# Kernel tuning notes

Hardware: AMD Instinct MI355X
Metric: run time of the kernel (lower is better)

The kernel has to match this reference:

```python
import jax, jax.numpy as jnp
import numpy as np

B, N, D = 2, 2048, 768
H = 12
HD = D // H
HID = 4 * D
SCALE = HD ** -0.5
EPS = 1e-5


def layer_norm(x, g, b):
    mu = jnp.mean(x, axis=-1, keepdims=True)
    var = jnp.var(x, axis=-1, keepdims=True)
    return (x - mu) * jax.lax.rsqrt(var + EPS) * g + b


def setup_inputs() -> dict:
    key = jax.random.key(0)
    ks = jax.random.split(key, 12)
    s = 0.02
    return {
        "x": jax.random.normal(ks[0], (B, N, D), jnp.float32),
        "att_mask": jax.random.randint(ks[1], (B, N), 0, 2, jnp.int32),
        "ln1_g": jnp.ones((D,), jnp.float32),
        "ln1_b": jnp.zeros((D,), jnp.float32),
        "qkv_w": jax.random.normal(ks[2], (3 * D, D), jnp.float32) * s,
        "q_bias": jnp.zeros((D,), jnp.float32),
        "v_bias": jnp.zeros((D,), jnp.float32),
        "proj_w": jax.random.normal(ks[3], (D, D), jnp.float32) * s,
        "proj_b": jnp.zeros((D,), jnp.float32),
        "ln2_g": jnp.ones((D,), jnp.float32),
        "ln2_b": jnp.zeros((D,), jnp.float32),
        "fc1_w": jax.random.normal(ks[4], (HID, D), jnp.float32) * s,
        "fc1_b": jnp.zeros((HID,), jnp.float32),
        "fc2_w": jax.random.normal(ks[5], (D, HID), jnp.float32) * s,
        "fc2_b": jnp.zeros((D,), jnp.float32),
        "gamma_1": 0.1 * jnp.ones((D,), jnp.float32),
        "gamma_2": 0.1 * jnp.ones((D,), jnp.float32),
    }


def reference(x, att_mask, ln1_g, ln1_b, qkv_w, q_bias, v_bias, proj_w, proj_b,
              ln2_g, ln2_b, fc1_w, fc1_b, fc2_w, fc2_b, gamma_1, gamma_2):
    # --- attention branch ---
    h = layer_norm(x, ln1_g, ln1_b)
    qkv_bias = jnp.concatenate([q_bias, jnp.zeros_like(v_bias), v_bias])
    qkv = h @ qkv_w.T + qkv_bias                      # [B,N,3D]
    qkv = qkv.reshape(B, N, 3, H, HD).transpose(2, 0, 3, 1, 4)
    q, k, v = qkv[0], qkv[1], qkv[2]                  # [B,H,N,HD]
    logit = jnp.einsum('bhqd,bhkd->bhqk', q * SCALE, k)
    mask = att_mask[:, None, None, :]                 # key mask [B,1,1,N]
    logit = jnp.where(mask == 0, -jnp.inf, logit)
    attn = jax.nn.softmax(logit, axis=-1)
    o = jnp.einsum('bhqk,bhkd->bhqd', attn, v)
    o = o.transpose(0, 2, 1, 3).reshape(B, N, D)
    o = o @ proj_w.T + proj_b
    x = x + gamma_1 * o
    # --- mlp branch ---
    h2 = layer_norm(x, ln2_g, ln2_b)
    h2 = jax.nn.gelu(h2 @ fc1_w.T + fc1_b, approximate=False)
    h2 = h2 @ fc2_w.T + fc2_b
    return x + gamma_2 * h2
```

## Files before the change

kernel.cpp:

```cpp
#include <hip/hip_runtime.h>
#include <hip/hip_bf16.h>
#include <stdint.h>

typedef __bf16 bf16x8 __attribute__((ext_vector_type(8)));
typedef __bf16 bf16x2 __attribute__((ext_vector_type(2)));
typedef unsigned short u16x8 __attribute__((ext_vector_type(8)));
typedef float f32x4 __attribute__((ext_vector_type(4)));
typedef float f32x16 __attribute__((ext_vector_type(16)));
typedef uint32_t u32x4 __attribute__((ext_vector_type(4)));

#define DMODEL 768
#define NSEQ   2048
#define BATCH  2
#define NHEAD  12
#define HDIM   64
#define HIDDEN 3072
#define PROWS  (BATCH * NHEAD * NSEQ)
#define QSCALE 0.18033688011112042f
#define MCONST 16.0f
#define PMASKED 1.52587890625e-05f

__device__ __forceinline__ uint16_t f2bf(float f) {
  __bf16 h = (__bf16)f;
  return __builtin_bit_cast(uint16_t, h);
}
__device__ __forceinline__ float bf2f(uint16_t u) {
  uint32_t x = (uint32_t)u << 16;
  return __builtin_bit_cast(float, x);
}
__device__ __forceinline__ bf16x8 ldb8(const uint16_t* p) {
  return __builtin_bit_cast(bf16x8, *reinterpret_cast<const u16x8*>(p));
}

using as1_void = __attribute__((address_space(1))) const void;
using as3_void = __attribute__((address_space(3))) void;
__device__ __forceinline__ void gload16(const uint16_t* src, uint16_t* lds) {
  __builtin_amdgcn_global_load_lds((as1_void*)src, (as3_void*)lds, 16, 0, 0);
}
#define MEMFENCE asm volatile("" ::: "memory")

#define N_QKVW  (3 * DMODEL * DMODEL)
#define N_PROJW (DMODEL * DMODEL)
#define N_FC1W  (HIDDEN * DMODEL)
#define N_FC2W  (DMODEL * HIDDEN)
__global__ __launch_bounds__(256) void cvt4_kernel(const float* __restrict__ s0,
                                                   const float* __restrict__ s1,
                                                   const float* __restrict__ s2,
                                                   const float* __restrict__ s3,
                                                   uint16_t* __restrict__ d0,
                                                   uint16_t* __restrict__ d1,
                                                   uint16_t* __restrict__ d2,
                                                   uint16_t* __restrict__ d3) {
  int i4 = (blockIdx.x * 256 + threadIdx.x) * 4;
  const float* s;
  uint16_t* d;
  if (i4 < N_QKVW) { s = s0 + i4; d = d0 + i4; }
  else if (i4 < N_QKVW + N_PROJW) { int j = i4 - N_QKVW; s = s1 + j; d = d1 + j; }
  else if (i4 < N_QKVW + N_PROJW + N_FC1W) { int j = i4 - N_QKVW - N_PROJW; s = s2 + j; d = d2 + j; }
  else { int j = i4 - N_QKVW - N_PROJW - N_FC1W; s = s3 + j; d = d3 + j; }
  float4 v = *reinterpret_cast<const float4*>(s);
  ushort4 o;
  o.x = f2bf(v.x); o.y = f2bf(v.y); o.z = f2bf(v.z); o.w = f2bf(v.w);
  *reinterpret_cast<ushort4*>(d) = o;
}

__global__ __launch_bounds__(256) void bias_kernel(const float* __restrict__ qb,
                                                   const float* __restrict__ vb,
                                                   float* __restrict__ out) {
  int j = blockIdx.x * 256 + threadIdx.x;
  if (j < 3 * DMODEL) {
    float v = 0.f;
    if (j < DMODEL) v = qb[j];
    else if (j >= 2 * DMODEL) v = vb[j - 2 * DMODEL];
    out[j] = v;
  }
}

__global__ __launch_bounds__(256) void ln_kernel(const float* __restrict__ x,
                                                 const float* __restrict__ g,
                                                 const float* __restrict__ bt,
                                                 uint16_t* __restrict__ out) {
  const int row = blockIdx.x;
  const int t = threadIdx.x;
  const float* xr = x + (size_t)row * DMODEL;
  float v0 = xr[t], v1 = xr[t + 256], v2 = xr[t + 512];
  float s = v0 + v1 + v2;
  float q = v0 * v0 + v1 * v1 + v2 * v2;
  for (int off = 32; off >= 1; off >>= 1) {
    s += __shfl_xor(s, off);
    q += __shfl_xor(q, off);
  }
  __shared__ float ss[4], sq[4];
  int w = t >> 6;
  if ((t & 63) == 0) { ss[w] = s; sq[w] = q; }
  __syncthreads();
  s = ss[0] + ss[1] + ss[2] + ss[3];
  q = sq[0] + sq[1] + sq[2] + sq[3];
  const float mean = s * (1.0f / DMODEL);
  const float var = q * (1.0f / DMODEL) - mean * mean;
  const float rstd = rsqrtf(var + 1e-5f);
  uint16_t* orow = out + (size_t)row * DMODEL;
  orow[t]       = f2bf((v0 - mean) * rstd * g[t]       + bt[t]);
  orow[t + 256] = f2bf((v1 - mean) * rstd * g[t + 256] + bt[t + 256]);
  orow[t + 512] = f2bf((v2 - mean) * rstd * g[t + 512] + bt[t + 512]);
}

template <int MODE>
__global__ __launch_bounds__(256, 3) void gemm128(const uint16_t* __restrict__ A,
                                                  const uint16_t* __restrict__ W,
                                                  const float* __restrict__ bias,
                                                  void* __restrict__ outp,
                                                  int M, int N, int K) {
  __shared__ uint16_t As[2][128 * 32];
  __shared__ uint16_t Bs[2][128 * 32];
  const int tid = threadIdx.x;
  const int lane = tid & 63;
  const int w = tid >> 6;
  const int wr = w >> 1, wc = w & 1;
  const int row0 = blockIdx.y * 128;
  const int col0 = blockIdx.x * 128;
  const int lr = lane & 15;
  const int g = lane >> 4;

  const int o0 = w * 1024 + lane * 16;
  const int o1 = o0 + 4096;
  const int r0s = o0 >> 6, c0s = (o0 & 63) >> 1;
  const int r1s = o1 >> 6, c1s = (o1 & 63) >> 1;
  const int l0 = (w * 1024) >> 1;
  const int l1 = l0 + 2048;
  const uint16_t* Abase = A + (size_t)row0 * K;
  const uint16_t* Wbase = W + (size_t)col0 * K;

  auto stage = [&](int kt) {
    uint16_t* Ad = &As[kt & 1][0];
    uint16_t* Bd = &Bs[kt & 1][0];
    const int kk = kt * 32;
    gload16(Abase + (size_t)r0s * K + kk + c0s, Ad + l0);
    gload16(Abase + (size_t)r1s * K + kk + c1s, Ad + l1);
    gload16(Wbase + (size_t)r0s * K + kk + c0s, Bd + l0);
    gload16(Wbase + (size_t)r1s * K + kk + c1s, Bd + l1);
  };

  f32x4 acc[4][4] = {};
  const int nt = K >> 5;
  stage(0);
  for (int kt = 0; kt < nt; ++kt) {
    if (kt + 1 < nt) {
      stage(kt + 1);
      asm volatile("s_waitcnt vmcnt(4)" ::: "memory");
    } else {
      asm volatile("s_waitcnt vmcnt(0)" ::: "memory");
    }
    __builtin_amdgcn_s_barrier();
    MEMFENCE;
    const uint16_t* Ab = &As[kt & 1][0];
    const uint16_t* Bb = &Bs[kt & 1][0];
    bf16x8 a[4], b[4];
#pragma unroll
    for (int m = 0; m < 4; ++m) a[m] = ldb8(Ab + (wr * 64 + m * 16 + lr) * 32 + g * 8);
#pragma unroll
    for (int n = 0; n < 4; ++n) b[n] = ldb8(Bb + (wc * 64 + n * 16 + lr) * 32 + g * 8);
#pragma unroll
    for (int m = 0; m < 4; ++m)
#pragma unroll
      for (int n = 0; n < 4; ++n)
        acc[m][n] = __builtin_amdgcn_mfma_f32_16x16x32_bf16(a[m], b[n], acc[m][n], 0, 0, 0);
    MEMFENCE;
    __builtin_amdgcn_s_barrier();
  }

#pragma unroll
  for (int m = 0; m < 4; ++m) {
    int row = row0 + wr * 64 + m * 16 + g * 4;
#pragma unroll
    for (int n = 0; n < 4; ++n) {
      int col = col0 + wc * 64 + n * 16 + lr;
      float bv = bias[col];
#pragma unroll
      for (int ri = 0; ri < 4; ++ri) {
        float val = acc[m][n][ri] + bv;
        size_t idx = (size_t)(row + ri) * N + col;
        if constexpr (MODE == 0) {
          if (col < DMODEL) val *= QSCALE;
          ((uint16_t*)outp)[idx] = f2bf(val);
        } else {
          float ge = 0.5f * val * (1.0f + erff(val * 0.70710678118654752f));
          ((uint16_t*)outp)[idx] = f2bf(ge);
        }
      }
    }
  }
}

__global__ __launch_bounds__(256, 3) void gemm64(const uint16_t* __restrict__ A,
                                                 const uint16_t* __restrict__ W,
                                                 const float* __restrict__ bias,
                                                 float* __restrict__ outp,
                                                 const float* __restrict__ resid,
                                                 const float* __restrict__ gamma,
                                                 int M, int N, int K) {
  __shared__ uint16_t As[2][64 * 64];
  __shared__ uint16_t Bs[2][64 * 64];
  const int tid = threadIdx.x;
  const int lane = tid & 63;
  const int w = tid >> 6;
  const int wr = w >> 1, wc = w & 1;
  const int row0 = blockIdx.y * 64;
  const int col0 = blockIdx.x * 64;
  const int lr = lane & 15;
  const int g = lane >> 4;

  const int srow = tid >> 3;
  const int schunk = tid & 7;
  const uint16_t* Abase = A + (size_t)row0 * K;
  const uint16_t* Wbase = W + (size_t)col0 * K;

  auto stage = [&](int kt) {
    uint16_t* Ad = &As[kt & 1][0];
    uint16_t* Bd = &Bs[kt & 1][0];
    const int kk = kt * 64;
#pragma unroll
    for (int i = 0; i < 2; ++i) {
      const int row = i * 32 + srow;
      const int sc = (schunk ^ (row & 7)) * 8;
      gload16(Abase + (size_t)row * K + kk + sc, Ad + i * 2048 + w * 512);
      gload16(Wbase + (size_t)row * K + kk + sc, Bd + i * 2048 + w * 512);
    }
  };

  f32x4 acc[2][2] = {};
  const int nt = K >> 6;
  stage(0);
  for (int kt = 0; kt < nt; ++kt) {
    if (kt + 1 < nt) {
      stage(kt + 1);
      asm volatile("s_waitcnt vmcnt(4)" ::: "memory");
    } else {
      asm volatile("s_waitcnt vmcnt(0)" ::: "memory");
    }
    __builtin_amdgcn_s_barrier();
    MEMFENCE;
    const uint16_t* Ab = &As[kt & 1][0];
    const uint16_t* Bb = &Bs[kt & 1][0];
#pragma unroll
    for (int kk = 0; kk < 2; ++kk) {
      bf16x8 a[2], bf[2];
#pragma unroll
      for (int m = 0; m < 2; ++m) {
        const int row = wr * 32 + m * 16 + lr;
        a[m] = ldb8(Ab + row * 64 + (((kk * 4 + g) ^ (row & 7)) * 8));
      }
#pragma unroll
      for (int n = 0; n < 2; ++n) {
        const int row = wc * 32 + n * 16 + lr;
        bf[n] = ldb8(Bb + row * 64 + (((kk * 4 + g) ^ (row & 7)) * 8));
      }
#pragma unroll
      for (int m = 0; m < 2; ++m)
#pragma unroll
        for (int n = 0; n < 2; ++n)
          acc[m][n] = __builtin_amdgcn_mfma_f32_16x16x32_bf16(a[m], bf[n], acc[m][n], 0, 0, 0);
    }
    MEMFENCE;
    __builtin_amdgcn_s_barrier();
  }

#pragma unroll
  for (int m = 0; m < 2; ++m) {
    int row = row0 + wr * 32 + m * 16 + g * 4;
#pragma unroll
    for (int n = 0; n < 2; ++n) {
      int col = col0 + wc * 32 + n * 16 + lr;
      float bv = bias[col];
      float gv = gamma[col];
#pragma unroll
      for (int ri = 0; ri < 4; ++ri) {
        float val = acc[m][n][ri] + bv;
        size_t idx = (size_t)(row + ri) * N + col;
        outp[idx] = resid[idx] + gv * val;
      }
    }
  }
}

__global__ __launch_bounds__(256) void prep_kernel(const uint16_t* __restrict__ qkv,
                                                   const int* __restrict__ mask,
                                                   uint16_t* __restrict__ km,
                                                   uint16_t* __restrict__ vt) {
  __shared__ uint16_t tile[64][72];
  const int t = threadIdx.x;
  const int bh = blockIdx.x;
  const int n0 = blockIdx.y * 64;
  const int b = bh / NHEAD, h = bh % NHEAD;
  const int* mb = mask + b * NSEQ;
  const uint16_t* src = qkv + (size_t)(b * NSEQ + n0) * (3 * DMODEL) + h * HDIM;
  uint16_t* kdst = km + (size_t)(b * NSEQ + n0) * DMODEL + h * HDIM;
#pragma unroll
  for (int it = 0; it < 2; ++it) {
    int slot = it * 256 + t;
    int r = slot >> 2, c = (slot & 3) * 16;
    uint16_t mz = (mb[n0 + r] != 0) ? (uint16_t)0xFFFF : (uint16_t)0;
    const uint16_t* rp = src + (size_t)r * (3 * DMODEL);
    u16x8 k0 = *reinterpret_cast<const u16x8*>(rp + DMODEL + c) & mz;
    u16x8 k1 = *reinterpret_cast<const u16x8*>(rp + DMODEL + c + 8) & mz;
    u16x8 v0 = *reinterpret_cast<const u16x8*>(rp + 2 * DMODEL + c) & mz;
    u16x8 v1 = *reinterpret_cast<const u16x8*>(rp + 2 * DMODEL + c + 8) & mz;
    *reinterpret_cast<u16x8*>(kdst + (size_t)r * DMODEL + c) = k0;
    *reinterpret_cast<u16x8*>(kdst + (size_t)r * DMODEL + c + 8) = k1;
    *reinterpret_cast<u16x8*>(&tile[r][c]) = v0;
    *reinterpret_cast<u16x8*>(&tile[r][c + 8]) = v1;
  }
  __syncthreads();
  uint16_t* dst = vt + (size_t)bh * HDIM * NSEQ + n0;
#pragma unroll
  for (int it = 0; it < 2; ++it) {
    int slot = it * 256 + t;
    int d = slot >> 2, c = (slot & 3) * 16;
    u16x8 a0, a1;
#pragma unroll
    for (int e = 0; e < 8; ++e) a0[e] = tile[c + e][d];
#pragma unroll
    for (int e = 0; e < 8; ++e) a1[e] = tile[c + 8 + e][d];
    *reinterpret_cast<u16x8*>(dst + (size_t)d * NSEQ + c) = a0;
    *reinterpret_cast<u16x8*>(dst + (size_t)d * NSEQ + c + 8) = a1;
  }
}

__global__ __launch_bounds__(256, 3) void attn_kernel(const uint16_t* __restrict__ qkv,
                                                      const uint16_t* __restrict__ km,
                                                      const uint16_t* __restrict__ vt,
                                                      const int* __restrict__ mask,
                                                      uint16_t* __restrict__ po,
                                                      float* __restrict__ pml) {
  __shared__ uint16_t Kb[2][64 * 64];
  __shared__ uint16_t Vb[2][64 * 64];
  __shared__ unsigned long long mbits[16];
  const int tid = threadIdx.x;
  const int lane = tid & 63;
  const int w = tid >> 6;
  const int bh = blockIdx.x;
  const int b = bh / NHEAD, hd = bh % NHEAD;
  const int z = blockIdx.z;
  const int kbase = z * 1024;
  const int q0 = blockIdx.y * 128 + w * 32;
  const int l31 = lane & 31;
  const int hh = lane >> 5;

  const int* mb = mask + b * NSEQ;
#pragma unroll
  for (int it = 0; it < 4; ++it) {
    unsigned long long bm = __ballot(mb[kbase + it * 256 + tid] != 0);
    if (lane == 0) mbits[it * 4 + w] = bm;
  }

  bf16x8 qa[4];
  const uint16_t* qptr = qkv + (size_t)(b * NSEQ + q0 + l31) * (3 * DMODEL) + hd * HDIM + hh * 8;
#pragma unroll
  for (int dblk = 0; dblk < 4; ++dblk) qa[dblk] = ldb8(qptr + dblk * 16);

  const uint16_t* kmb = km + (size_t)b * NSEQ * DMODEL + hd * HDIM;
  const uint16_t* vtb = vt + (size_t)bh * HDIM * NSEQ;

  __syncthreads();

  const int srow = tid >> 3;
  const int sxor = ((tid & 7) ^ (srow & 7)) * 8;
  auto stage = [&](int t) {
    const int pb = t & 1;
    const int k0 = kbase + t * 64;
#pragma unroll
    for (int i = 0; i < 2; ++i) {
      const int row = i * 32 + srow;
      gload16(kmb + (size_t)(k0 + row) * DMODEL + sxor, &Kb[pb][i * 2048 + w * 512]);
      gload16(vtb + (size_t)row * NSEQ + k0 + sxor, &Vb[pb][i * 2048 + w * 512]);
    }
  };

  u16x8 ones_u;
#pragma unroll
  for (int e = 0; e < 8; ++e) ones_u[e] = 0x3F80;
  const bf16x8 ones = __builtin_bit_cast(bf16x8, ones_u);

  f32x16 oacc[2] = {};
  f32x16 lacc = {};

  stage(0);
  for (int t = 0; t < 16; ++t) {
    if (t + 1 < 16) {
      stage(t + 1);
      asm volatile("s_waitcnt vmcnt(4)" ::: "memory");
    } else {
      asm volatile("s_waitcnt vmcnt(0)" ::: "memory");
    }
    __builtin_amdgcn_s_barrier();
    MEMFENCE;
    const uint16_t* Kbp = &Kb[t & 1][0];
    const uint16_t* Vbp = &Vb[t & 1][0];

    f32x16 st[2];
    __builtin_amdgcn_s_setprio(1);
#pragma unroll
    for (int kblk = 0; kblk < 2; ++kblk) {
      f32x16 acc = {};
      const uint16_t* kr = Kbp + (kblk * 32 + l31) * 64;
#pragma unroll
      for (int dblk = 0; dblk < 4; ++dblk) {
        bf16x8 kf = ldb8(kr + ((dblk * 2 + hh) ^ (l31 & 7)) * 8);
        acc = __builtin_amdgcn_mfma_f32_32x32x16_bf16(kf, qa[dblk], acc, 0, 0, 0);
      }
      st[kblk] = acc;
    }
    __builtin_amdgcn_s_setprio(0);

    uint32_t pk[2][8];
#pragma unroll
    for (int kblk = 0; kblk < 2; ++kblk)
#pragma unroll
      for (int wn = 0; wn < 8; ++wn) {
        float e0 = exp2f(st[kblk][2 * wn] - MCONST);
        float e1 = exp2f(st[kblk][2 * wn + 1] - MCONST);
        bf16x2 pr = {(__bf16)e0, (__bf16)e1};
        pk[kblk][wn] = __builtin_bit_cast(uint32_t, pr);
      }

    bf16x8 af[4];
#pragma unroll
    for (int kb16 = 0; kb16 < 4; ++kb16) {
      const int kblk = kb16 >> 1;
      const int a4 = (kb16 & 1) * 4;
      uint32_t ow0 = hh ? pk[kblk][a4 + 2] : pk[kblk][a4 + 0];
      uint32_t ow1 = hh ? pk[kblk][a4 + 3] : pk[kblk][a4 + 1];
      uint32_t gv0 = hh ? pk[kblk][a4 + 0] : pk[kblk][a4 + 2];
      uint32_t gv1 = hh ? pk[kblk][a4 + 1] : pk[kblk][a4 + 3];
      uint32_t sw0 = (uint32_t)__shfl_xor((int)gv0, 32);
      uint32_t sw1 = (uint32_t)__shfl_xor((int)gv1, 32);
      u32x4 afu;
      afu[0] = hh ? sw0 : ow0;
      afu[1] = hh ? sw1 : ow1;
      afu[2] = hh ? ow0 : sw0;
      afu[3] = hh ? ow1 : sw1;
      af[kb16] = __builtin_bit_cast(bf16x8, afu);
    }

    __builtin_amdgcn_s_setprio(1);
#pragma unroll
    for (int dblk = 0; dblk < 2; ++dblk) {
      const uint16_t* vr = Vbp + (dblk * 32 + l31) * 64;
#pragma unroll
      for (int kb16 = 0; kb16 < 4; ++kb16) {
        bf16x8 vf = ldb8(vr + ((kb16 * 2 + hh) ^ (l31 & 7)) * 8);
        oacc[dblk] = __builtin_amdgcn_mfma_f32_32x32x16_bf16(af[kb16], vf, oacc[dblk], 0, 0, 0);
      }
    }
#pragma unroll
    for (int kb16 = 0; kb16 < 4; ++kb16)
      lacc = __builtin_amdgcn_mfma_f32_32x32x16_bf16(af[kb16], ones, lacc, 0, 0, 0);
    __builtin_amdgcn_s_setprio(0);
    MEMFENCE;
    __builtin_amdgcn_s_barrier();
  }

  int cnt = 0;
#pragma unroll
  for (int it = 0; it < 16; ++it) cnt += 64 - __popcll(mbits[it]);
  const float cntf = (float)cnt * PMASKED;

  uint16_t* ob = po + ((size_t)z * PROWS + (size_t)bh * NSEQ + q0) * 64;
#pragma unroll
  for (int r = 0; r < 16; ++r) {
    const int qrow = (r & 3) + 8 * (r >> 2) + 4 * hh;
#pragma unroll
    for (int dblk = 0; dblk < 2; ++dblk)
      ob[(size_t)qrow * 64 + dblk * 32 + l31] = f2bf(oacc[dblk][r]);
  }
  if (l31 == 0) {
#pragma unroll
    for (int r = 0; r < 16; ++r) {
      const int qrow = (r & 3) + 8 * (r >> 2) + 4 * hh;
      pml[(size_t)z * PROWS + (size_t)bh * NSEQ + q0 + qrow] = lacc[r] - cntf;
    }
  }
}

__global__ __launch_bounds__(256) void merge_kernel(const uint16_t* __restrict__ po,
                                                    const float* __restrict__ pml,
                                                    uint16_t* __restrict__ o) {
  int gid = blockIdx.x * 256 + threadIdx.x;
  int row = gid >> 3;
  int c0 = (gid & 7) * 8;
  float L = pml[row] + pml[PROWS + row];
  float inv = L > 0.f ? 1.f / L : 0.f;
  u16x8 a = *reinterpret_cast<const u16x8*>(po + (size_t)row * 64 + c0);
  u16x8 b = *reinterpret_cast<const u16x8*>(po + ((size_t)PROWS + row) * 64 + c0);
  int bh = row >> 11, q = row & 2047;
  int bb = bh / NHEAD, hh = bh % NHEAD;
  uint16_t* op = o + ((size_t)(bb * NSEQ + q) * DMODEL + hh * HDIM + c0);
  u16x8 outv;
#pragma unroll
  for (int e = 0; e < 8; ++e)
    outv[e] = f2bf((bf2f(a[e]) + bf2f(b[e])) * inv);
  *reinterpret_cast<u16x8*>(op) = outv;
}

extern "C" void kernel_launch(void* const* d_in, const int* in_sizes, int n_in,
                              void* d_out, int out_size, void* d_ws, size_t ws_size,
                              hipStream_t stream) {
  const float* x      = (const float*)d_in[0];
  const int*   amask  = (const int*)d_in[1];
  const float* ln1_g  = (const float*)d_in[2];
  const float* ln1_b  = (const float*)d_in[3];
  const float* qkv_w  = (const float*)d_in[4];
  const float* q_bias = (const float*)d_in[5];
  const float* v_bias = (const float*)d_in[6];
  const float* proj_w = (const float*)d_in[7];
  const float* proj_b = (const float*)d_in[8];
  const float* ln2_g  = (const float*)d_in[9];
  const float* ln2_b  = (const float*)d_in[10];
  const float* fc1_w  = (const float*)d_in[11];
  const float* fc1_b  = (const float*)d_in[12];
  const float* fc2_w  = (const float*)d_in[13];
  const float* fc2_b  = (const float*)d_in[14];
  const float* g1     = (const float*)d_in[15];
  const float* g2     = (const float*)d_in[16];

  char* ws = (char*)d_ws;
  uint16_t* qkvw_bf  = (uint16_t*)(ws + 0);
  uint16_t* projw_bf = (uint16_t*)(ws + 3538944);
  uint16_t* fc1w_bf  = (uint16_t*)(ws + 4718592);
  uint16_t* fc2w_bf  = (uint16_t*)(ws + 9437184);
  float*    qkvbias  = (float*)(ws + 14155776);
  uint16_t* h_bf     = (uint16_t*)(ws + 14164992);
  uint16_t* km       = h_bf;
  uint16_t* h2_bf    = h_bf;
  uint16_t* qkv_bf   = (uint16_t*)(ws + 20456448);
  uint16_t* vt_bf    = (uint16_t*)(ws + 39330816);
  uint16_t* o_bf     = (uint16_t*)(ws + 45622272);
  float*    x1_f     = (float*)(ws + 51913728);
  uint16_t* po       = (uint16_t*)(ws + 51913728);
  float*    pml      = (float*)(ws + 64496640);
  uint16_t* fc1_bf   = qkv_bf;

  const int M = BATCH * NSEQ;

  cvt4_kernel<<<(N_QKVW + N_PROJW + N_FC1W + N_FC2W) / 1024, 256, 0, stream>>>(
      qkv_w, proj_w, fc1_w, fc2_w, qkvw_bf, projw_bf, fc1w_bf, fc2w_bf);
  bias_kernel<<<(3 * DMODEL + 255) / 256, 256, 0, stream>>>(q_bias, v_bias, qkvbias);

  ln_kernel<<<M, 256, 0, stream>>>(x, ln1_g, ln1_b, h_bf);
  gemm128<0><<<dim3((3 * DMODEL) / 128, M / 128), 256, 0, stream>>>(
      h_bf, qkvw_bf, qkvbias, qkv_bf, M, 3 * DMODEL, DMODEL);
  prep_kernel<<<dim3(BATCH * NHEAD, NSEQ / 64), 256, 0, stream>>>(qkv_bf, amask, km, vt_bf);
  attn_kernel<<<dim3(BATCH * NHEAD, NSEQ / 128, 2), 256, 0, stream>>>(
      qkv_bf, km, vt_bf, amask, po, pml);
  merge_kernel<<<(PROWS * 8) / 256, 256, 0, stream>>>(po, pml, o_bf);
  gemm64<<<dim3(DMODEL / 64, M / 64), 256, 0, stream>>>(
      o_bf, projw_bf, proj_b, x1_f, x, g1, M, DMODEL, DMODEL);
  ln_kernel<<<M, 256, 0, stream>>>(x1_f, ln2_g, ln2_b, h2_bf);
  gemm128<2><<<dim3(HIDDEN / 128, M / 128), 256, 0, stream>>>(
      h2_bf, fc1w_bf, fc1_b, fc1_bf, M, HIDDEN, DMODEL);
  gemm64<<<dim3(DMODEL / 64, M / 64), 256, 0, stream>>>(
      fc1_bf, fc2w_bf, fc2_b, (float*)d_out, x1_f, g2, M, DMODEL, HIDDEN);
}
```

Before: 195.2 us.

## Fuse K/V masking and V transpose into QKV GEMM; split attention keys four ways

The QKV GEMM epilogue now writes Q, the masked K, and the masked, transposed V directly, which removes the separate prep kernel and its round trip through global memory. The attention kernel moves to 512-thread blocks covering 256 queries, and the key range is split into four chunks of 512 keys instead of two chunks of 1024. The merge kernel sums four partial outputs. The V-transpose stores from the GEMM epilogue are scattered 8-byte writes, and the four-way split adds more partial-output traffic in the merge.

```diff
diff --git a/kernel.cpp b/kernel.cpp
--- a/kernel.cpp
+++ b/kernel.cpp
@@ -16,6 +16,7 @@
 #define HDIM   64
 #define HIDDEN 3072
 #define PROWS  (BATCH * NHEAD * NSEQ)
+#define NZ     4
 #define QSCALE 0.18033688011112042f
 #define MCONST 16.0f
 #define PMASKED 1.52587890625e-05f
@@ -110,6 +111,9 @@
                                                   const uint16_t* __restrict__ W,
                                                   const float* __restrict__ bias,
                                                   void* __restrict__ outp,
+                                                  uint16_t* __restrict__ km,
+                                                  uint16_t* __restrict__ vt,
+                                                  const int* __restrict__ amask,
                                                   int M, int N, int K) {
   __shared__ uint16_t As[2][128 * 32];
   __shared__ uint16_t Bs[2][128 * 32];
@@ -169,23 +173,58 @@
     __builtin_amdgcn_s_barrier();
   }
 
-#pragma unroll
-  for (int m = 0; m < 4; ++m) {
-    int row = row0 + wr * 64 + m * 16 + g * 4;
-#pragma unroll
-    for (int n = 0; n < 4; ++n) {
-      int col = col0 + wc * 64 + n * 16 + lr;
-      float bv = bias[col];
-#pragma unroll
-      for (int ri = 0; ri < 4; ++ri) {
-        float val = acc[m][n][ri] + bv;
-        size_t idx = (size_t)(row + ri) * N + col;
-        if constexpr (MODE == 0) {
-          if (col < DMODEL) val *= QSCALE;
-          ((uint16_t*)outp)[idx] = f2bf(val);
+  if constexpr (MODE == 0) {
+    const int sect = col0 / DMODEL;
+    const int bb = row0 >> 11;
+    const int* mrow = amask + bb * NSEQ;
+#pragma unroll
+    for (int m = 0; m < 4; ++m) {
+      int row = row0 + wr * 64 + m * 16 + g * 4;
+      int nn = row & 2047;
+      int mk[4];
+#pragma unroll
+      for (int ri = 0; ri < 4; ++ri) mk[ri] = mrow[nn + ri];
+#pragma unroll
+      for (int n = 0; n < 4; ++n) {
+        int col = col0 + wc * 64 + n * 16 + lr;
+        float bv = bias[col];
+        if (sect == 0) {
+#pragma unroll
+          for (int ri = 0; ri < 4; ++ri)
+            ((uint16_t*)outp)[(size_t)(row + ri) * DMODEL + col] =
+                f2bf((acc[m][n][ri] + bv) * QSCALE);
+        } else if (sect == 1) {
+          int kc = col - DMODEL;
+#pragma unroll
+          for (int ri = 0; ri < 4; ++ri)
+            km[(size_t)(row + ri) * DMODEL + kc] =
+                mk[ri] ? f2bf(acc[m][n][ri] + bv) : (uint16_t)0;
         } else {
+          int vc = col - 2 * DMODEL;
+          int hh2 = vc >> 6, dd = vc & 63;
+          ushort4 sv;
+          sv.x = mk[0] ? f2bf(acc[m][n][0] + bv) : (uint16_t)0;
+          sv.y = mk[1] ? f2bf(acc[m][n][1] + bv) : (uint16_t)0;
+          sv.z = mk[2] ? f2bf(acc[m][n][2] + bv) : (uint16_t)0;
+          sv.w = mk[3] ? f2bf(acc[m][n][3] + bv) : (uint16_t)0;
+          *reinterpret_cast<ushort4*>(
+              vt + ((size_t)((bb * NHEAD + hh2) * 64 + dd)) * NSEQ + nn) = sv;
+        }
+      }
+    }
+  } else {
+#pragma unroll
+    for (int m = 0; m < 4; ++m) {
+      int row = row0 + wr * 64 + m * 16 + g * 4;
+#pragma unroll
+      for (int n = 0; n < 4; ++n) {
+        int col = col0 + wc * 64 + n * 16 + lr;
+        float bv = bias[col];
+#pragma unroll
+        for (int ri = 0; ri < 4; ++ri) {
+          float val = acc[m][n][ri] + bv;
           float ge = 0.5f * val * (1.0f + erff(val * 0.70710678118654752f));
-          ((uint16_t*)outp)[idx] = f2bf(ge);
+          ((uint16_t*)outp)[(size_t)(row + ri) * N + col] = f2bf(ge);
         }
       }
     }
@@ -283,50 +322,7 @@
   }
 }
 
-__global__ __launch_bounds__(256) void prep_kernel(const uint16_t* __restrict__ qkv,
-                                                   const int* __restrict__ mask,
-                                                   uint16_t* __restrict__ km,
-                                                   uint16_t* __restrict__ vt) {
-  __shared__ uint16_t tile[64][72];
-  const int t = threadIdx.x;
-  const int bh = blockIdx.x;
-  const int n0 = blockIdx.y * 64;
-  const int b = bh / NHEAD, h = bh % NHEAD;
-  const int* mb = mask + b * NSEQ;
-  const uint16_t* src = qkv + (size_t)(b * NSEQ + n0) * (3 * DMODEL) + h * HDIM;
-  uint16_t* kdst = km + (size_t)(b * NSEQ + n0) * DMODEL + h * HDIM;
-#pragma unroll
-  for (int it = 0; it < 2; ++it) {
-    int slot = it * 256 + t;
-    int r = slot >> 2, c = (slot & 3) * 16;
-    uint16_t mz = (mb[n0 + r] != 0) ? (uint16_t)0xFFFF : (uint16_t)0;
-    const uint16_t* rp = src + (size_t)r * (3 * DMODEL);
-    u16x8 k0 = *reinterpret_cast<const u16x8*>(rp + DMODEL + c) & mz;
-    u16x8 k1 = *reinterpret_cast<const u16x8*>(rp + DMODEL + c + 8) & mz;
-    u16x8 v0 = *reinterpret_cast<const u16x8*>(rp + 2 * DMODEL + c) & mz;
-    u16x8 v1 = *reinterpret_cast<const u16x8*>(rp + 2 * DMODEL + c + 8) & mz;
-    *reinterpret_cast<u16x8*>(kdst + (size_t)r * DMODEL + c) = k0;
-    *reinterpret_cast<u16x8*>(kdst + (size_t)r * DMODEL + c + 8) = k1;
-    *reinterpret_cast<u16x8*>(&tile[r][c]) = v0;
-    *reinterpret_cast<u16x8*>(&tile[r][c + 8]) = v1;
-  }
-  __syncthreads();
-  uint16_t* dst = vt + (size_t)bh * HDIM * NSEQ + n0;
-#pragma unroll
-  for (int it = 0; it < 2; ++it) {
-    int slot = it * 256 + t;
-    int d = slot >> 2, c = (slot & 3) * 16;
-    u16x8 a0, a1;
-#pragma unroll
-    for (int e = 0; e < 8; ++e) a0[e] = tile[c + e][d];
-#pragma unroll
-    for (int e = 0; e < 8; ++e) a1[e] = tile[c + 8 + e][d];
-    *reinterpret_cast<u16x8*>(dst + (size_t)d * NSEQ + c) = a0;
-    *reinterpret_cast<u16x8*>(dst + (size_t)d * NSEQ + c + 8) = a1;
-  }
-}
-
-__global__ __launch_bounds__(256, 3) void attn_kernel(const uint16_t* __restrict__ qkv,
+__global__ __launch_bounds__(512, 6) void attn_kernel(const uint16_t* __restrict__ qb_,
                                                       const uint16_t* __restrict__ km,
                                                       const uint16_t* __restrict__ vt,
                                                       const int* __restrict__ mask,
@@ -334,27 +330,26 @@
                                                       float* __restrict__ pml) {
   __shared__ uint16_t Kb[2][64 * 64];
   __shared__ uint16_t Vb[2][64 * 64];
-  __shared__ unsigned long long mbits[16];
+  __shared__ unsigned long long mbits[8];
   const int tid = threadIdx.x;
   const int lane = tid & 63;
   const int w = tid >> 6;
   const int bh = blockIdx.x;
   const int b = bh / NHEAD, hd = bh % NHEAD;
   const int z = blockIdx.z;
-  const int kbase = z * 1024;
-  const int q0 = blockIdx.y * 128 + w * 32;
+  const int kbase = z * 512;
+  const int q0 = blockIdx.y * 256 + w * 32;
   const int l31 = lane & 31;
   const int hh = lane >> 5;
 
   const int* mb = mask + b * NSEQ;
-#pragma unroll
-  for (int it = 0; it < 4; ++it) {
-    unsigned long long bm = __ballot(mb[kbase + it * 256 + tid] != 0);
-    if (lane == 0) mbits[it * 4 + w] = bm;
+  {
+    unsigned long long bm = __ballot(mb[kbase + w * 64 + lane] != 0);
+    if (lane == 0) mbits[w] = bm;
   }
 
   bf16x8 qa[4];
-  const uint16_t* qptr = qkv + (size_t)(b * NSEQ + q0 + l31) * (3 * DMODEL) + hd * HDIM + hh * 8;
+  const uint16_t* qptr = qb_ + (size_t)(b * NSEQ + q0 + l31) * DMODEL + hd * HDIM + hh * 8;
 #pragma unroll
   for (int dblk = 0; dblk < 4; ++dblk) qa[dblk] = ldb8(qptr + dblk * 16);
 
@@ -368,12 +363,8 @@
   auto stage = [&](int t) {
     const int pb = t & 1;
     const int k0 = kbase + t * 64;
-#pragma unroll
-    for (int i = 0; i < 2; ++i) {
-      const int row = i * 32 + srow;
-      gload16(kmb + (size_t)(k0 + row) * DMODEL + sxor, &Kb[pb][i * 2048 + w * 512]);
-      gload16(vtb + (size_t)row * NSEQ + k0 + sxor, &Vb[pb][i * 2048 + w * 512]);
-    }
+    gload16(kmb + (size_t)(k0 + srow) * DMODEL + sxor, &Kb[pb][w * 512]);
+    gload16(vtb + (size_t)srow * NSEQ + k0 + sxor, &Vb[pb][w * 512]);
   };
 
   u16x8 ones_u;
@@ -385,10 +376,10 @@
   f32x16 lacc = {};
 
   stage(0);
-  for (int t = 0; t < 16; ++t) {
-    if (t + 1 < 16) {
+  for (int t = 0; t < 8; ++t) {
+    if (t + 1 < 8) {
       stage(t + 1);
-      asm volatile("s_waitcnt vmcnt(4)" ::: "memory");
+      asm volatile("s_waitcnt vmcnt(2)" ::: "memory");
     } else {
       asm volatile("s_waitcnt vmcnt(0)" ::: "memory");
     }
@@ -462,7 +453,7 @@
 
   int cnt = 0;
 #pragma unroll
-  for (int it = 0; it < 16; ++it) cnt += 64 - __popcll(mbits[it]);
+  for (int it = 0; it < 8; ++it) cnt += 64 - __popcll(mbits[it]);
   const float cntf = (float)cnt * PMASKED;
 
   uint16_t* ob = po + ((size_t)z * PROWS + (size_t)bh * NSEQ + q0) * 64;
@@ -488,17 +479,23 @@
   int gid = blockIdx.x * 256 + threadIdx.x;
   int row = gid >> 3;
   int c0 = (gid & 7) * 8;
-  float L = pml[row] + pml[PROWS + row];
+  float L = 0.f;
+#pragma unroll
+  for (int zz = 0; zz < NZ; ++zz) L += pml[(size_t)zz * PROWS + row];
   float inv = L > 0.f ? 1.f / L : 0.f;
-  u16x8 a = *reinterpret_cast<const u16x8*>(po + (size_t)row * 64 + c0);
-  u16x8 b = *reinterpret_cast<const u16x8*>(po + ((size_t)PROWS + row) * 64 + c0);
+  float sum[8] = {};
+#pragma unroll
+  for (int zz = 0; zz < NZ; ++zz) {
+    u16x8 a = *reinterpret_cast<const u16x8*>(po + ((size_t)zz * PROWS + row) * 64 + c0);
+#pragma unroll
+    for (int e = 0; e < 8; ++e) sum[e] += bf2f(a[e]);
+  }
   int bh = row >> 11, q = row & 2047;
   int bb = bh / NHEAD, hh = bh % NHEAD;
   uint16_t* op = o + ((size_t)(bb * NSEQ + q) * DMODEL + hh * HDIM + c0);
   u16x8 outv;
 #pragma unroll
-  for (int e = 0; e < 8; ++e)
-    outv[e] = f2bf((bf2f(a[e]) + bf2f(b[e])) * inv);
+  for (int e = 0; e < 8; ++e) outv[e] = f2bf(sum[e] * inv);
   *reinterpret_cast<u16x8*>(op) = outv;
 }
 
@@ -530,15 +527,15 @@
   uint16_t* fc2w_bf  = (uint16_t*)(ws + 9437184);
   float*    qkvbias  = (float*)(ws + 14155776);
   uint16_t* h_bf     = (uint16_t*)(ws + 14164992);
-  uint16_t* km       = h_bf;
+  uint16_t* q_bf     = (uint16_t*)(ws + 20456448);
+  uint16_t* km       = (uint16_t*)(ws + 26747904);
+  uint16_t* vt_bf    = (uint16_t*)(ws + 33039360);
+  uint16_t* po       = (uint16_t*)(ws + 39330816);
+  float*    pml      = (float*)(ws + 64496640);
+  uint16_t* o_bf     = q_bf;
+  float*    x1_f     = (float*)(ws + 26747904);
+  uint16_t* fc1_bf   = (uint16_t*)(ws + 39330816);
   uint16_t* h2_bf    = h_bf;
-  uint16_t* qkv_bf   = (uint16_t*)(ws + 20456448);
-  uint16_t* vt_bf    = (uint16_t*)(ws + 39330816);
-  uint16_t* o_bf     = (uint16_t*)(ws + 45622272);
-  float*    x1_f     = (float*)(ws + 51913728);
-  uint16_t* po       = (uint16_t*)(ws + 51913728);
-  float*    pml      = (float*)(ws + 64496640);
-  uint16_t* fc1_bf   = qkv_bf;
 
   const int M = BATCH * NSEQ;
 
@@ -548,16 +545,15 @@
 
   ln_kernel<<<M, 256, 0, stream>>>(x, ln1_g, ln1_b, h_bf);
   gemm128<0><<<dim3((3 * DMODEL) / 128, M / 128), 256, 0, stream>>>(
-      h_bf, qkvw_bf, qkvbias, qkv_bf, M, 3 * DMODEL, DMODEL);
-  prep_kernel<<<dim3(BATCH * NHEAD, NSEQ / 64), 256, 0, stream>>>(qkv_bf, amask, km, vt_bf);
-  attn_kernel<<<dim3(BATCH * NHEAD, NSEQ / 128, 2), 256, 0, stream>>>(
-      qkv_bf, km, vt_bf, amask, po, pml);
+      h_bf, qkvw_bf, qkvbias, q_bf, km, vt_bf, amask, M, 3 * DMODEL, DMODEL);
+  attn_kernel<<<dim3(BATCH * NHEAD, NSEQ / 256, NZ), 512, 0, stream>>>(
+      q_bf, km, vt_bf, amask, po, pml);
   merge_kernel<<<(PROWS * 8) / 256, 256, 0, stream>>>(po, pml, o_bf);
   gemm64<<<dim3(DMODEL / 64, M / 64), 256, 0, stream>>>(
       o_bf, projw_bf, proj_b, x1_f, x, g1, M, DMODEL, DMODEL);
   ln_kernel<<<M, 256, 0, stream>>>(x1_f, ln2_g, ln2_b, h2_bf);
   gemm128<2><<<dim3(HIDDEN / 128, M / 128), 256, 0, stream>>>(
-      h2_bf, fc1w_bf, fc1_b, fc1_bf, M, HIDDEN, DMODEL);
+      h2_bf, fc1w_bf, fc1_b, fc1_bf, nullptr, nullptr, nullptr, M, HIDDEN, DMODEL);
   gemm64<<<dim3(DMODEL / 64, M / 64), 256, 0, stream>>>(
       fc1_bf, fc2w_bf, fc2_b, (float*)d_out, x1_f, g2, M, DMODEL, HIDDEN);
 }
```

New measurement: 343.0 us. +75.7%, slower.
